# Optimization experiments

Hardware: AMD Instinct MI355X
Metric: run time of the kernel (lower is better)

Reference implementation:

```python
import jax, jax.numpy as jnp
import numpy as np

N3, F = 25000, 64
V2, V1, V0 = 100000, 400000, 1600000


def _unique_idx(key, n_src, n_dst):
    # cluster-centre positions: n_src unique indices in [0, n_dst)
    return jax.random.permutation(key, n_dst)[:n_src].reshape(n_src, 1).astype(jnp.int32)


def setup_inputs() -> dict:
    key = jax.random.key(0)
    kx, k0, k1, k2 = jax.random.split(key, 4)
    x = jax.random.normal(kx, (N3, F), dtype=jnp.float32)
    idx2 = _unique_idx(k2, N3, V2)   # [25000, 1] -> positions in V2
    idx1 = _unique_idx(k1, V2, V1)   # [100000, 1] -> positions in V1
    idx0 = _unique_idx(k0, V1, V0)   # [400000, 1] -> positions in V0
    return {"x": x, "idx0": idx0, "idx1": idx1, "idx2": idx2,
            "v0": V0, "v1": V1, "v2": V2}


def _backscatter(x, idx, v):
    # tf.scatter_nd(idx [N,1], x [N,F], [v,F]) == zeros.at[idx[:,0]].add(x)
    return jnp.zeros((v, x.shape[1]), x.dtype).at[idx[:, 0]].add(x)


def reference(x, idx0, idx1, idx2, v0, v1, v2):
    # scatters list is processed in reverse: deepest clustering undone first
    x = _backscatter(x, idx2, v2)   # [V2, F]
    x = _backscatter(x, idx1, v1)   # [V1, F]
    x = _backscatter(x, idx0, v0)   # [V0, F]
    return x
```

## Files before the change

### kernel.cpp

```cpp
#include <hip/hip_runtime.h>


__global__ void zero_out_kernel(float4* __restrict__ out, long n4) {
    long i = (long)blockIdx.x * blockDim.x + threadIdx.x;
    if (i < n4) {
        out[i] = make_float4(0.f, 0.f, 0.f, 0.f);
    }
}

__global__ void scatter_rows_kernel(const float4* __restrict__ x,
                                    const int* __restrict__ idx0,
                                    const int* __restrict__ idx1,
                                    const int* __restrict__ idx2,
                                    float4* __restrict__ out,
                                    int n3) {
    int t = blockIdx.x * blockDim.x + threadIdx.x;
    int row = t >> 4;
    int c   = t & 15;
    if (row >= n3) return;
    int j2 = idx2[row];
    int j1 = idx1[j2];
    int j0 = idx0[j1];
    out[(long)j0 * 16 + c] = x[(long)row * 16 + c];
}

extern "C" void kernel_launch(void* const* d_in, const int* in_sizes, int n_in,
                              void* d_out, int out_size, void* d_ws, size_t ws_size,
                              hipStream_t stream) {
    const float* x    = (const float*)d_in[0];
    const int*   idx0 = (const int*)d_in[1];
    const int*   idx1 = (const int*)d_in[2];
    const int*   idx2 = (const int*)d_in[3];
    float* out = (float*)d_out;

    const int n3 = in_sizes[3];

    long n4 = (long)out_size / 4;
    int  zblocks = (int)((n4 + 255) / 256);
    zero_out_kernel<<<zblocks, 256, 0, stream>>>((float4*)out, n4);

    int total = n3 * 16;
    int sblocks = (total + 255) / 256;
    scatter_rows_kernel<<<sblocks, 256, 0, stream>>>(
        (const float4*)x, idx0, idx1, idx2, (float4*)out, n3);
}
```

Baseline: 407.0 us.

## Replace zero-then-scatter with inverse-index map and single gather write pass

Builds an inverse map from output row to input row in workspace by composing the three index levels, then writes every output row once. Each row gets either the gathered input row or zeros, using non-temporal stores. This removes the separate zeroing pass followed by random scatter writes. It adds an init and build pass plus an extra indirect load per output vector, and it relies on the indices being unique.

```diff
diff --git a/kernel.cpp b/kernel.cpp
--- a/kernel.cpp
+++ b/kernel.cpp
@@ -1,27 +1,41 @@
 #include <hip/hip_runtime.h>
 
 
-__global__ void zero_out_kernel(float4* __restrict__ out, long n4) {
-    long i = (long)blockIdx.x * blockDim.x + threadIdx.x;
-    if (i < n4) {
-        out[i] = make_float4(0.f, 0.f, 0.f, 0.f);
+typedef float f32x4 __attribute__((ext_vector_type(4)));
+typedef int   i32x4 __attribute__((ext_vector_type(4)));
+
+
+__global__ void init_inv_kernel(i32x4* __restrict__ inv4, int n) {
+    int i = blockIdx.x * blockDim.x + threadIdx.x;
+    if (i < n) {
+        i32x4 m = {-1, -1, -1, -1};
+        inv4[i] = m;
     }
 }
 
-__global__ void scatter_rows_kernel(const float4* __restrict__ x,
-                                    const int* __restrict__ idx0,
-                                    const int* __restrict__ idx1,
-                                    const int* __restrict__ idx2,
-                                    float4* __restrict__ out,
-                                    int n3) {
-    int t = blockIdx.x * blockDim.x + threadIdx.x;
-    int row = t >> 4;
-    int c   = t & 15;
-    if (row >= n3) return;
-    int j2 = idx2[row];
-    int j1 = idx1[j2];
-    int j0 = idx0[j1];
-    out[(long)j0 * 16 + c] = x[(long)row * 16 + c];
+__global__ void build_inv_kernel(const int* __restrict__ idx0,
+                                 const int* __restrict__ idx1,
+                                 const int* __restrict__ idx2,
+                                 int* __restrict__ inv, int n3) {
+    int i = blockIdx.x * blockDim.x + threadIdx.x;
+    if (i < n3) {
+        int j2 = idx2[i];
+        int j1 = idx1[j2];
+        int j0 = idx0[j1];
+        inv[j0] = i;
+    }
+}
+
+__global__ void write_out_kernel(const f32x4* __restrict__ x,
+                                 const int* __restrict__ inv,
+                                 f32x4* __restrict__ out,
+                                 long n4) {
+    long i = (long)blockIdx.x * blockDim.x + threadIdx.x;
+    if (i >= n4) return;
+    int r = inv[i >> 4];
+    f32x4 v = {0.f, 0.f, 0.f, 0.f};
+    if (r >= 0) v = x[(long)r * 16 + (i & 15)];
+    __builtin_nontemporal_store(v, &out[i]);
 }
 
 extern "C" void kernel_launch(void* const* d_in, const int* in_sizes, int n_in,
@@ -34,13 +48,17 @@
     float* out = (float*)d_out;
 
     const int n3 = in_sizes[3];
+    const int F  = in_sizes[0] / n3;
+    const int v0 = out_size / F;
+
+    int* inv = (int*)d_ws;
+
+    int n_i4 = v0 / 4;
+    init_inv_kernel<<<(n_i4 + 255) / 256, 256, 0, stream>>>((i32x4*)inv, n_i4);
+
+    build_inv_kernel<<<(n3 + 255) / 256, 256, 0, stream>>>(idx0, idx1, idx2, inv, n3);
 
     long n4 = (long)out_size / 4;
-    int  zblocks = (int)((n4 + 255) / 256);
-    zero_out_kernel<<<zblocks, 256, 0, stream>>>((float4*)out, n4);
-
-    int total = n3 * 16;
-    int sblocks = (total + 255) / 256;
-    scatter_rows_kernel<<<sblocks, 256, 0, stream>>>(
-        (const float4*)x, idx0, idx1, idx2, (float4*)out, n3);
+    write_out_kernel<<<(int)((n4 + 255) / 256), 256, 0, stream>>>(
+        (const f32x4*)x, inv, (f32x4*)out, n4);
 }
```

Result: slower. 442.3 us (+8.7%).
